# Performance work log

Measured on AMD Instinct MI355X. Metric: run time of the kernel, lower is better.

The kernel has to match this reference:

```python
import jax, jax.numpy as jnp
import numpy as np

N_NODES = 50000
N_EDGES = 1600000
N_GRAPHS = 64
IN_DIM = 128
HID = 128
N_CLASSES = 10


def setup_inputs() -> dict:
    key = jax.random.key(0)
    ks = jax.random.split(key, 12)
    x = jax.random.normal(ks[0], (N_NODES, IN_DIM), dtype=jnp.float32)
    edge_index = jax.random.randint(ks[1], (2, N_EDGES), 0, N_NODES, dtype=jnp.int32)
    batch = jnp.sort(jax.random.randint(ks[2], (N_NODES,), 0, N_GRAPHS, dtype=jnp.int32))
    def glorot(k, shape):
        s = 1.0 / np.sqrt(shape[0])
        return jax.random.uniform(k, shape, jnp.float32, -s, s)
    W1 = glorot(ks[3], (IN_DIM, HID)); b1 = jnp.zeros((HID,), jnp.float32)
    W2 = glorot(ks[4], (HID, HID));    b2 = jnp.zeros((HID,), jnp.float32)
    Wc1 = glorot(ks[5], (HID, HID));   bc1 = glorot(ks[6], (HID,))
    Wc2 = glorot(ks[7], (HID, N_CLASSES)); bc2 = glorot(ks[8], (N_CLASSES,))
    return {"x": x, "edge_index": edge_index, "batch": batch,
            "W1": W1, "b1": b1, "W2": W2, "b2": b2,
            "Wc1": Wc1, "bc1": bc1, "Wc2": Wc2, "bc2": bc2}


def gcn_conv(x, edge_index, W, b):
    """PyG GCNConv: sym-normalized A-hat (with self loops) @ (x W) + b."""
    n = x.shape[0]
    loop = jnp.arange(n, dtype=edge_index.dtype)
    src = jnp.concatenate([edge_index[0], loop])  # message source
    dst = jnp.concatenate([edge_index[1], loop])  # message target
    deg = jax.ops.segment_sum(jnp.ones_like(src, dtype=x.dtype), dst, num_segments=n)
    dinv = jnp.where(deg > 0, jax.lax.rsqrt(deg), jnp.zeros_like(deg))
    norm = dinv[src] * dinv[dst]  # [E+N]
    h = x @ W                     # [N, H]
    msg = h[src] * norm[:, None]  # gather + scale
    out = jax.ops.segment_sum(msg, dst, num_segments=n)
    return out + b


def reference(x, edge_index, batch, W1, b1, W2, b2, Wc1, bc1, Wc2, bc2):
    h = jax.nn.relu(gcn_conv(x, edge_index, W1, b1))
    h = jax.nn.relu(gcn_conv(h, edge_index, W2, b2))
    # per-graph mean pooling (segment mean)
    sums = jax.ops.segment_sum(h, batch, num_segments=N_GRAPHS)
    cnt = jax.ops.segment_sum(jnp.ones((h.shape[0],), h.dtype), batch, num_segments=N_GRAPHS)
    g = sums / jnp.clip(cnt, 1.0)[:, None]  # [G, H]
    z = jax.nn.relu(g @ Wc1 + bc1)
    return z @ Wc2 + bc2
```

## Files before the change

kernel.cpp:

```cpp
#include <hip/hip_runtime.h>
#include <cstdint>
#include <cstddef>

#define CHUNK 4096

typedef __attribute__((ext_vector_type(8))) short short8;
typedef __attribute__((ext_vector_type(4))) float f32x4;

__device__ __forceinline__ float bf2f(unsigned short u) {
  return __uint_as_float(((unsigned)u) << 16);
}
__device__ __forceinline__ unsigned short f2bf(float f) {
  unsigned u = __float_as_uint(f);
  u += 0x7fffu + ((u >> 16) & 1u);
  return (unsigned short)(u >> 16);
}

__global__ void transpose2_w_k(const float* __restrict__ W1, const float* __restrict__ W2,
                               unsigned short* __restrict__ W1t, unsigned short* __restrict__ W2t) {
  int idx = blockIdx.x * 256 + threadIdx.x;
  const float* W = (idx < 16384) ? W1 : W2;
  unsigned short* Wt = (idx < 16384) ? W1t : W2t;
  int i = idx & 16383;
  int k = i >> 7, n = i & 127;
  Wt[n * 128 + k] = f2bf(W[i]);
}

__global__ void count_edges_k(const int* __restrict__ dst, int E, int* __restrict__ cnt) {
  int e = blockIdx.x * blockDim.x + threadIdx.x;
  if (e < E) atomicAdd(&cnt[dst[e]], 1);
}

__global__ void dinv_k(const int* __restrict__ cnt, float* __restrict__ dinv, int n) {
  int i = blockIdx.x * blockDim.x + threadIdx.x;
  if (i < n) dinv[i] = rsqrtf((float)cnt[i] + 1.0f);
}

template <typename CT>
__global__ void fill_csr_k(const int* __restrict__ src, const int* __restrict__ dst, int E,
                           int* __restrict__ cursor, CT* __restrict__ col) {
  int e = blockIdx.x * blockDim.x + threadIdx.x;
  if (e < E) {
    int d = dst[e], s = src[e];
    int pos = atomicAdd(&cursor[d], 1);
    col[pos] = (CT)s;
  }
}

__global__ void scan1_k(const int* __restrict__ cnt, int* __restrict__ rs,
                        int* __restrict__ partials, int n) {
  __shared__ int s[1024];
  int t = threadIdx.x;
  int gid = blockIdx.x * 1024 + t;
  int v = (gid < n) ? cnt[gid] : 0;
  s[t] = v;
  __syncthreads();
  for (int off = 1; off < 1024; off <<= 1) {
    int u = (t >= off) ? s[t - off] : 0;
    __syncthreads();
    s[t] += u;
    __syncthreads();
  }
  if (gid < n) rs[gid] = s[t] - v;
  if (t == 1023) partials[blockIdx.x] = s[1023];
}

__global__ void scan2_k(int* __restrict__ partials, int nb) {
  if (threadIdx.x == 0 && blockIdx.x == 0) {
    int acc = 0;
    for (int i = 0; i < nb; i++) { int v = partials[i]; partials[i] = acc; acc += v; }
  }
}

__global__ void scan3_k(int* __restrict__ rs, int* __restrict__ cursor,
                        const int* __restrict__ partials, int n, int total) {
  int gid = blockIdx.x * blockDim.x + threadIdx.x;
  if (gid < n) {
    int v = rs[gid] + partials[gid >> 10];
    rs[gid] = v;
    cursor[gid] = v;
  }
  if (gid == 0) rs[n] = total;
}

__global__ __launch_bounds__(256) void scatter_atomic_k(const int* __restrict__ src,
                                                        const int* __restrict__ dst, int E,
                                                        int* __restrict__ gcur,
                                                        unsigned int* __restrict__ tmp,
                                                        int cap, int B) {
  __shared__ unsigned pk[CHUNK];
  __shared__ unsigned char bk[CHUNK];
  __shared__ int h[256];
  __shared__ int cur[256];
  __shared__ int base_s[256];
  int t = threadIdx.x;
  h[t] = 0;
  __syncthreads();
  int e0 = blockIdx.x * CHUNK;
  int e1 = e0 + CHUNK; if (e1 > E) e1 = E;
  int m = e1 - e0;
  for (int i = t; i < m; i += 256) {
    int d = dst[e0 + i], s = src[e0 + i];
    int b = d >> 8;
    pk[i] = ((unsigned)s << 8) | (unsigned)(d & 255);
    bk[i] = (unsigned char)b;
    atomicAdd(&h[b], 1);
  }
  __syncthreads();
  if (t < B && h[t] > 0) base_s[t] = atomicAdd(&gcur[t], h[t]);
  cur[t] = 0;
  __syncthreads();
  for (int i = t; i < m; i += 256) {
    int b = bk[i];
    int r = atomicAdd(&cur[b], 1);
    int p = base_s[b] + r;
    if (p < cap) tmp[(size_t)b * cap + p] = pk[i];
  }
}

__global__ void base2_k(const int* __restrict__ gcur, int B, int cap,
                        int* __restrict__ bucket_base) {
  int lane = threadIdx.x;
  int running = 0;
  for (int c0 = 0; c0 < B; c0 += 64) {
    int idx = c0 + lane;
    int cb = (idx < B) ? gcur[idx] : 0;
    if (cb > cap) cb = cap;
    int v = cb;
    #pragma unroll
    for (int off = 1; off < 64; off <<= 1) {
      int u = __shfl_up(v, off);
      if (lane >= off) v += u;
    }
    int tot = __shfl(v, 63);
    if (idx < B) bucket_base[idx] = running + (v - cb);
    running += tot;
  }
  if (lane == 0) bucket_base[B] = running;
}

__global__ __launch_bounds__(256) void cntfill2_k(const unsigned int* __restrict__ tmp,
                                                  const int* __restrict__ gcur,
                                                  const int* __restrict__ bucket_base,
                                                  int N, int E, int cap,
                                                  float* __restrict__ dinv,
                                                  int* __restrict__ rs,
                                                  unsigned short* __restrict__ col) {
  __shared__ int c[256];
  __shared__ int cur[256];
  int b = blockIdx.x, t = threadIdx.x;
  c[t] = 0;
  __syncthreads();
  int cnt_b = gcur[b]; if (cnt_b > cap) cnt_b = cap;
  const unsigned* tb = tmp + (size_t)b * cap;
  for (int i = t; i < cnt_b; i += 256) atomicAdd(&c[tb[i] & 255u], 1);
  __syncthreads();
  int v = c[t];
  cur[t] = v;
  __syncthreads();
  for (int off = 1; off < 256; off <<= 1) {
    int u = (t >= off) ? cur[t - off] : 0;
    __syncthreads();
    cur[t] += u;
    __syncthreads();
  }
  int rsv = bucket_base[b] + cur[t] - v;
  int node = (b << 8) + t;
  if (node < N) {
    rs[node] = rsv;
    dinv[node] = rsqrtf((float)v + 1.0f);
  }
  if (b == 0 && t == 0) rs[N] = E;
  __syncthreads();
  cur[t] = rsv;
  __syncthreads();
  for (int i = t; i < cnt_b; i += 256) {
    unsigned u = tb[i];
    int pos = atomicAdd(&cur[u & 255u], 1);
    col[pos] = (unsigned short)(u >> 8);
  }
}

template <bool AF32>
__global__ __launch_bounds__(256) void gemm_bf_k(const void* __restrict__ Ap,
                                                 const unsigned short* __restrict__ Wt,
                                                 unsigned short* __restrict__ C, int N) {
  __shared__ unsigned short Ws[128 * 136];
  for (int idx = threadIdx.x; idx < 2048; idx += 256) {
    int n = idx >> 4, c = idx & 15;
    *(uint4*)&Ws[n * 136 + c * 8] = ((const uint4*)Wt)[idx];
  }
  __syncthreads();
  const int w = threadIdx.x >> 6;
  const int lane = threadIdx.x & 63;
  const int quad = lane >> 4, l16 = lane & 15;
  const int rb = blockIdx.x * 128 + w * 32;
  f32x4 acc[2][8] = {};
  #pragma unroll
  for (int ks = 0; ks < 4; ks++) {
    short8 aF[2];
    #pragma unroll
    for (int m = 0; m < 2; m++) {
      int r = rb + m * 16 + l16;
      short8 a = {};
      if (r < N) {
        if (AF32) {
          const float* ar = (const float*)Ap + (size_t)r * 128 + ks * 32 + quad * 8;
          float4 u0 = *(const float4*)ar;
          float4 u1 = *(const float4*)(ar + 4);
          a[0] = (short)f2bf(u0.x); a[1] = (short)f2bf(u0.y);
          a[2] = (short)f2bf(u0.z); a[3] = (short)f2bf(u0.w);
          a[4] = (short)f2bf(u1.x); a[5] = (short)f2bf(u1.y);
          a[6] = (short)f2bf(u1.z); a[7] = (short)f2bf(u1.w);
        } else {
          a = *(const short8*)((const unsigned short*)Ap + (size_t)r * 128 + ks * 32 + quad * 8);
        }
      }
      aF[m] = a;
    }
    #pragma unroll
    for (int t = 0; t < 8; t++) {
      short8 bF = *(const short8*)&Ws[(t * 16 + l16) * 136 + ks * 32 + quad * 8];
      acc[0][t] = __builtin_amdgcn_mfma_f32_16x16x32_bf16(aF[0], bF, acc[0][t], 0, 0, 0);
      acc[1][t] = __builtin_amdgcn_mfma_f32_16x16x32_bf16(aF[1], bF, acc[1][t], 0, 0, 0);
    }
  }
  __syncthreads();
  unsigned short* Cs = Ws;
  #pragma unroll
  for (int m = 0; m < 2; m++) {
    int rloc = w * 32 + m * 16 + quad * 4;
    #pragma unroll
    for (int t = 0; t < 8; t++)
      #pragma unroll
      for (int rg = 0; rg < 4; rg++)
        Cs[(rloc + rg) * 132 + t * 16 + l16] = f2bf(acc[m][t][rg]);
  }
  __syncthreads();
  const int r0 = blockIdx.x * 128;
  for (int idx = threadIdx.x; idx < 2048; idx += 256) {
    int row = idx >> 4, c = idx & 15;
    int rr = r0 + row;
    if (rr < N) {
      uint2 a = *(uint2*)&Cs[row * 132 + c * 8];
      uint2 b = *(uint2*)&Cs[row * 132 + c * 8 + 4];
      ((uint4*)C)[(size_t)rr * 16 + c] = make_uint4(a.x, a.y, b.x, b.y);
    }
  }
}

template <typename CT>
__global__ __launch_bounds__(256) void agg8_k(const unsigned short* __restrict__ h,
                                              const int* __restrict__ rs,
                                              const CT* __restrict__ col,
                                              const float* __restrict__ dinv,
                                              const float* __restrict__ bias,
                                              unsigned short* __restrict__ outp, int n) {
  int wid = (blockIdx.x * blockDim.x + threadIdx.x) >> 6;
  int lane = threadIdx.x & 63;
  if (wid >= n) return;
  const int g = lane >> 4;
  const int l = lane & 15;
  float di = dinv[wid];
  float acc[8];
  {
    uint4 sv = ((const uint4*)(h + (size_t)wid * 128))[l];
    float ws = (g == 0) ? di : 0.f;
    acc[0] = bf2f((unsigned short)sv.x) * ws;
    acc[1] = bf2f((unsigned short)(sv.x >> 16)) * ws;
    acc[2] = bf2f((unsigned short)sv.y) * ws;
    acc[3] = bf2f((unsigned short)(sv.y >> 16)) * ws;
    acc[4] = bf2f((unsigned short)sv.z) * ws;
    acc[5] = bf2f((unsigned short)(sv.z >> 16)) * ws;
    acc[6] = bf2f((unsigned short)sv.w) * ws;
    acc[7] = bf2f((unsigned short)(sv.w >> 16)) * ws;
  }
  int beg = rs[wid], end = rs[wid + 1];
  for (int base = beg; base < end; base += 8) {
    int e0 = base + g, e1 = base + 4 + g;
    int i0 = (e0 < end) ? e0 : end - 1;
    int i1 = (e1 < end) ? e1 : end - 1;
    int s0 = (int)col[i0], s1 = (int)col[i1];
    float w0 = (e0 < end) ? dinv[s0] : 0.f;
    float w1 = (e1 < end) ? dinv[s1] : 0.f;
    uint4 h0 = ((const uint4*)(h + (size_t)s0 * 128))[l];
    uint4 h1 = ((const uint4*)(h + (size_t)s1 * 128))[l];
    acc[0] += bf2f((unsigned short)h0.x) * w0 + bf2f((unsigned short)h1.x) * w1;
    acc[1] += bf2f((unsigned short)(h0.x >> 16)) * w0 + bf2f((unsigned short)(h1.x >> 16)) * w1;
    acc[2] += bf2f((unsigned short)h0.y) * w0 + bf2f((unsigned short)h1.y) * w1;
    acc[3] += bf2f((unsigned short)(h0.y >> 16)) * w0 + bf2f((unsigned short)(h1.y >> 16)) * w1;
    acc[4] += bf2f((unsigned short)h0.z) * w0 + bf2f((unsigned short)h1.z) * w1;
    acc[5] += bf2f((unsigned short)(h0.z >> 16)) * w0 + bf2f((unsigned short)(h1.z >> 16)) * w1;
    acc[6] += bf2f((unsigned short)h0.w) * w0 + bf2f((unsigned short)h1.w) * w1;
    acc[7] += bf2f((unsigned short)(h0.w >> 16)) * w0 + bf2f((unsigned short)(h1.w >> 16)) * w1;
  }
  #pragma unroll
  for (int j = 0; j < 8; j++) {
    acc[j] += __shfl_xor(acc[j], 16);
    acc[j] += __shfl_xor(acc[j], 32);
  }
  if (g == 0) {
    float4 bA = *(const float4*)(bias + l * 8);
    float4 bB = *(const float4*)(bias + l * 8 + 4);
    float r0 = fmaxf(acc[0] * di + bA.x, 0.f);
    float r1 = fmaxf(acc[1] * di + bA.y, 0.f);
    float r2 = fmaxf(acc[2] * di + bA.z, 0.f);
    float r3 = fmaxf(acc[3] * di + bA.w, 0.f);
    float r4 = fmaxf(acc[4] * di + bB.x, 0.f);
    float r5 = fmaxf(acc[5] * di + bB.y, 0.f);
    float r6 = fmaxf(acc[6] * di + bB.z, 0.f);
    float r7 = fmaxf(acc[7] * di + bB.w, 0.f);
    uint4 v;
    v.x = (unsigned)f2bf(r0) | ((unsigned)f2bf(r1) << 16);
    v.y = (unsigned)f2bf(r2) | ((unsigned)f2bf(r3) << 16);
    v.z = (unsigned)f2bf(r4) | ((unsigned)f2bf(r5) << 16);
    v.w = (unsigned)f2bf(r6) | ((unsigned)f2bf(r7) << 16);
    ((uint4*)outp)[(size_t)wid * 16 + l] = v;
  }
}

__global__ void poolb_k(const unsigned short* __restrict__ h, const int* __restrict__ batch, int n,
                        float* __restrict__ pool, float* __restrict__ gcnt) {
  int f = threadIdx.x;
  int n0 = blockIdx.x * 64;
  if (n0 >= n) return;
  int n1 = n0 + 64; if (n1 > n) n1 = n;
  int gcur = batch[n0];
  float acc = 0.f, cacc = 0.f;
  for (int i = n0; i < n1; i++) {
    int g = batch[i];
    if (g != gcur) {
      atomicAdd(&pool[gcur * 128 + f], acc);
      if (f == 0) atomicAdd(&gcnt[gcur], cacc);
      acc = 0.f; cacc = 0.f; gcur = g;
    }
    acc += bf2f(h[(size_t)i * 128 + f]);
    cacc += 1.f;
  }
  atomicAdd(&pool[gcur * 128 + f], acc);
  if (f == 0) atomicAdd(&gcnt[gcur], cacc);
}

__global__ void classify_k(const float* __restrict__ pool, const float* __restrict__ gcnt,
                           const float* __restrict__ Wc1, const float* __restrict__ bc1,
                           const float* __restrict__ Wc2, const float* __restrict__ bc2,
                           float* __restrict__ out, int nc) {
  __shared__ float gs[128];
  __shared__ float zs[128];
  int g = blockIdx.x, t = threadIdx.x;
  float c = gcnt[g]; if (c < 1.f) c = 1.f;
  gs[t] = pool[g * 128 + t] / c;
  __syncthreads();
  float acc = bc1[t];
  for (int k = 0; k < 128; k++) acc += gs[k] * Wc1[k * 128 + t];
  zs[t] = fmaxf(acc, 0.f);
  __syncthreads();
  if (t < nc) {
    float o = bc2[t];
    for (int k = 0; k < 128; k++) o += zs[k] * Wc2[k * nc + t];
    out[g * nc + t] = o;
  }
}

extern "C" void kernel_launch(void* const* d_in, const int* in_sizes, int n_in,
                              void* d_out, int out_size, void* d_ws, size_t ws_size,
                              hipStream_t stream) {
  const float* x   = (const float*)d_in[0];
  const int*   ei  = (const int*)d_in[1];
  const int*   bat = (const int*)d_in[2];
  const float* W1  = (const float*)d_in[3];
  const float* b1  = (const float*)d_in[4];
  const float* W2  = (const float*)d_in[5];
  const float* b2  = (const float*)d_in[6];
  const float* Wc1 = (const float*)d_in[7];
  const float* bc1 = (const float*)d_in[8];
  const float* Wc2 = (const float*)d_in[9];
  const float* bc2 = (const float*)d_in[10];
  float* out = (float*)d_out;

  const int N  = in_sizes[0] / 128;
  const int E  = in_sizes[1] / 2;
  const int NC = in_sizes[10];
  const int G  = out_size / NC;
  const int* src = ei;
  const int* dst = ei + E;
  (void)n_in; (void)ws_size;

  size_t off = 0;
  auto walloc = [&](size_t bytes) -> void* {
    void* p = (char*)d_ws + off;
    off += (bytes + 255) & ~(size_t)255;
    return p;
  };
  unsigned short* B2 = (unsigned short*)walloc((size_t)N * 128 * 2);
  unsigned short* B3 = (unsigned short*)walloc((size_t)N * 128 * 2);
  unsigned short* W1t = (unsigned short*)walloc(128 * 128 * 2);
  unsigned short* W2t = (unsigned short*)walloc(128 * 128 * 2);
  float* dinv = (float*)walloc((size_t)N * 4);
  int*   rs   = (int*)  walloc((size_t)(N + 1) * 4);
  float* pool = (float*)walloc((size_t)G * 129 * 4);
  float* gcnt = pool + (size_t)G * 128;

  const bool small = (N <= 65535);
  const int gblocks = (N + 127) / 128;
  const int aggGrid = (N + 3) / 4;

  transpose2_w_k<<<128, 256, 0, stream>>>(W1, W2, W1t, W2t);

  if (small) {
    const int B    = (N + 255) >> 8;
    const int nblk = (E + CHUNK - 1) / CHUNK;
    const int cap  = (E + B - 1) / B + 2048;
    unsigned short* col = (unsigned short*)walloc((size_t)E * 2);
    unsigned int*   tmp = (unsigned int*)  walloc((size_t)B * cap * 4);
    int* gcur        = (int*)walloc((size_t)B * 4);
    int* bucket_base = (int*)walloc((size_t)(B + 1) * 4);

    hipMemsetAsync(gcur, 0, (size_t)B * 4, stream);
    scatter_atomic_k<<<nblk, 256, 0, stream>>>(src, dst, E, gcur, tmp, cap, B);
    base2_k<<<1, 64, 0, stream>>>(gcur, B, cap, bucket_base);
    cntfill2_k<<<B, 256, 0, stream>>>(tmp, gcur, bucket_base, N, E, cap, dinv, rs, col);

    gemm_bf_k<true><<<gblocks, 256, 0, stream>>>(x, W1t, B2, N);
    agg8_k<unsigned short><<<aggGrid, 256, 0, stream>>>(B2, rs, col, dinv, b1, B3, N);
    gemm_bf_k<false><<<gblocks, 256, 0, stream>>>(B3, W2t, B2, N);
    agg8_k<unsigned short><<<aggGrid, 256, 0, stream>>>(B2, rs, col, dinv, b2, B3, N);
  } else {
    const int nb = (N + 1023) / 1024;
    int* cnt    = (int*)walloc((size_t)N * 4);
    int* cursor = (int*)walloc((size_t)N * 4);
    int* col    = (int*)walloc((size_t)E * 4);
    int* partials = (int*)walloc(256 * 4);
    hipMemsetAsync(cnt, 0, (size_t)N * 4, stream);
    count_edges_k<<<(E + 255) / 256, 256, 0, stream>>>(dst, E, cnt);
    scan1_k<<<nb, 1024, 0, stream>>>(cnt, rs, partials, N);
    scan2_k<<<1, 64, 0, stream>>>(partials, nb);
    scan3_k<<<(N + 255) / 256, 256, 0, stream>>>(rs, cursor, partials, N, E);
    dinv_k<<<(N + 255) / 256, 256, 0, stream>>>(cnt, dinv, N);
    fill_csr_k<int><<<(E + 255) / 256, 256, 0, stream>>>(src, dst, E, cursor, col);

    gemm_bf_k<true><<<gblocks, 256, 0, stream>>>(x, W1t, B2, N);
    agg8_k<int><<<aggGrid, 256, 0, stream>>>(B2, rs, col, dinv, b1, B3, N);
    gemm_bf_k<false><<<gblocks, 256, 0, stream>>>(B3, W2t, B2, N);
    agg8_k<int><<<aggGrid, 256, 0, stream>>>(B2, rs, col, dinv, b2, B3, N);
  }

  hipMemsetAsync(pool, 0, (size_t)G * 129 * 4, stream);
  poolb_k<<<(N + 63) / 64, 128, 0, stream>>>(B3, bat, N, pool, gcnt);
  classify_k<<<G, 128, 0, stream>>>(pool, gcnt, Wc1, bc1, Wc2, bc2, out, NC);
}
```

Before: 314.4 us.

## Fuse CSR build with first GEMM and merge pooling with classifier

Several launches are merged. The gcur memset goes into the weight-transpose kernel, and the bucket-base scan moves into each CSR-fill block. CSR fill and the first GEMM share one grid through a shared-memory union. Pooling plus classifier become one per-graph kernel that binary-searches the sorted batch array, so atomics and the pool memset disappear. This cuts launch overhead and lets the CSR fill overlap the GEMM, but only 64 blocks now do the pooling, and the sequential sum per graph may be slow.

Result: slower. 384.3 us (+22.2%).

```diff
diff --git a/kernel.cpp b/kernel.cpp
--- a/kernel.cpp
+++ b/kernel.cpp
@@ -16,71 +16,21 @@
   return (unsigned short)(u >> 16);
 }
 
-__global__ void transpose2_w_k(const float* __restrict__ W1, const float* __restrict__ W2,
-                               unsigned short* __restrict__ W1t, unsigned short* __restrict__ W2t) {
+union SMem {
+  unsigned short ws[128 * 136];
+  struct { int c[256]; int cur[256]; int sb[256]; } cf;
+};
+
+__global__ void prep_k(const float* __restrict__ W1, const float* __restrict__ W2,
+                       unsigned short* __restrict__ W1t, unsigned short* __restrict__ W2t,
+                       int* __restrict__ gcur, int B) {
   int idx = blockIdx.x * 256 + threadIdx.x;
   const float* W = (idx < 16384) ? W1 : W2;
   unsigned short* Wt = (idx < 16384) ? W1t : W2t;
   int i = idx & 16383;
   int k = i >> 7, n = i & 127;
   Wt[n * 128 + k] = f2bf(W[i]);
-}
-
-__global__ void count_edges_k(const int* __restrict__ dst, int E, int* __restrict__ cnt) {
-  int e = blockIdx.x * blockDim.x + threadIdx.x;
-  if (e < E) atomicAdd(&cnt[dst[e]], 1);
-}
-
-__global__ void dinv_k(const int* __restrict__ cnt, float* __restrict__ dinv, int n) {
-  int i = blockIdx.x * blockDim.x + threadIdx.x;
-  if (i < n) dinv[i] = rsqrtf((float)cnt[i] + 1.0f);
-}
-
-template <typename CT>
-__global__ void fill_csr_k(const int* __restrict__ src, const int* __restrict__ dst, int E,
-                           int* __restrict__ cursor, CT* __restrict__ col) {
-  int e = blockIdx.x * blockDim.x + threadIdx.x;
-  if (e < E) {
-    int d = dst[e], s = src[e];
-    int pos = atomicAdd(&cursor[d], 1);
-    col[pos] = (CT)s;
-  }
-}
-
-__global__ void scan1_k(const int* __restrict__ cnt, int* __restrict__ rs,
-                        int* __restrict__ partials, int n) {
-  __shared__ int s[1024];
-  int t = threadIdx.x;
-  int gid = blockIdx.x * 1024 + t;
-  int v = (gid < n) ? cnt[gid] : 0;
-  s[t] = v;
-  __syncthreads();
-  for (int off = 1; off < 1024; off <<= 1) {
-    int u = (t >= off) ? s[t - off] : 0;
-    __syncthreads();
-    s[t] += u;
-    __syncthreads();
-  }
-  if (gid < n) rs[gid] = s[t] - v;
-  if (t == 1023) partials[blockIdx.x] = s[1023];
-}
-
-__global__ void scan2_k(int* __restrict__ partials, int nb) {
-  if (threadIdx.x == 0 && blockIdx.x == 0) {
-    int acc = 0;
-    for (int i = 0; i < nb; i++) { int v = partials[i]; partials[i] = acc; acc += v; }
-  }
-}
-
-__global__ void scan3_k(int* __restrict__ rs, int* __restrict__ cursor,
-                        const int* __restrict__ partials, int n, int total) {
-  int gid = blockIdx.x * blockDim.x + threadIdx.x;
-  if (gid < n) {
-    int v = rs[gid] + partials[gid >> 10];
-    rs[gid] = v;
-    cursor[gid] = v;
-  }
-  if (gid == 0) rs[n] = total;
+  if (blockIdx.x == 0 && threadIdx.x < B) gcur[threadIdx.x] = 0;
 }
 
 __global__ __launch_bounds__(256) void scatter_atomic_k(const int* __restrict__ src,
@@ -118,83 +68,19 @@
   }
 }
 
-__global__ void base2_k(const int* __restrict__ gcur, int B, int cap,
-                        int* __restrict__ bucket_base) {
-  int lane = threadIdx.x;
-  int running = 0;
-  for (int c0 = 0; c0 < B; c0 += 64) {
-    int idx = c0 + lane;
-    int cb = (idx < B) ? gcur[idx] : 0;
-    if (cb > cap) cb = cap;
-    int v = cb;
-    #pragma unroll
-    for (int off = 1; off < 64; off <<= 1) {
-      int u = __shfl_up(v, off);
-      if (lane >= off) v += u;
-    }
-    int tot = __shfl(v, 63);
-    if (idx < B) bucket_base[idx] = running + (v - cb);
-    running += tot;
-  }
-  if (lane == 0) bucket_base[B] = running;
-}
-
-__global__ __launch_bounds__(256) void cntfill2_k(const unsigned int* __restrict__ tmp,
-                                                  const int* __restrict__ gcur,
-                                                  const int* __restrict__ bucket_base,
-                                                  int N, int E, int cap,
-                                                  float* __restrict__ dinv,
-                                                  int* __restrict__ rs,
-                                                  unsigned short* __restrict__ col) {
-  __shared__ int c[256];
-  __shared__ int cur[256];
-  int b = blockIdx.x, t = threadIdx.x;
-  c[t] = 0;
-  __syncthreads();
-  int cnt_b = gcur[b]; if (cnt_b > cap) cnt_b = cap;
-  const unsigned* tb = tmp + (size_t)b * cap;
-  for (int i = t; i < cnt_b; i += 256) atomicAdd(&c[tb[i] & 255u], 1);
-  __syncthreads();
-  int v = c[t];
-  cur[t] = v;
-  __syncthreads();
-  for (int off = 1; off < 256; off <<= 1) {
-    int u = (t >= off) ? cur[t - off] : 0;
-    __syncthreads();
-    cur[t] += u;
-    __syncthreads();
-  }
-  int rsv = bucket_base[b] + cur[t] - v;
-  int node = (b << 8) + t;
-  if (node < N) {
-    rs[node] = rsv;
-    dinv[node] = rsqrtf((float)v + 1.0f);
-  }
-  if (b == 0 && t == 0) rs[N] = E;
-  __syncthreads();
-  cur[t] = rsv;
-  __syncthreads();
-  for (int i = t; i < cnt_b; i += 256) {
-    unsigned u = tb[i];
-    int pos = atomicAdd(&cur[u & 255u], 1);
-    col[pos] = (unsigned short)(u >> 8);
-  }
-}
-
 template <bool AF32>
-__global__ __launch_bounds__(256) void gemm_bf_k(const void* __restrict__ Ap,
-                                                 const unsigned short* __restrict__ Wt,
-                                                 unsigned short* __restrict__ C, int N) {
-  __shared__ unsigned short Ws[128 * 136];
+__device__ __forceinline__ void gemm_tile(SMem& sm, const void* Ap,
+                                          const unsigned short* Wt,
+                                          unsigned short* C, int N, int tile) {
   for (int idx = threadIdx.x; idx < 2048; idx += 256) {
     int n = idx >> 4, c = idx & 15;
-    *(uint4*)&Ws[n * 136 + c * 8] = ((const uint4*)Wt)[idx];
+    *(uint4*)&sm.ws[n * 136 + c * 8] = ((const uint4*)Wt)[idx];
   }
   __syncthreads();
   const int w = threadIdx.x >> 6;
   const int lane = threadIdx.x & 63;
   const int quad = lane >> 4, l16 = lane & 15;
-  const int rb = blockIdx.x * 128 + w * 32;
+  const int rb = tile * 128 + w * 32;
   f32x4 acc[2][8] = {};
   #pragma unroll
   for (int ks = 0; ks < 4; ks++) {
@@ -220,13 +106,13 @@
     }
     #pragma unroll
     for (int t = 0; t < 8; t++) {
-      short8 bF = *(const short8*)&Ws[(t * 16 + l16) * 136 + ks * 32 + quad * 8];
+      short8 bF = *(const short8*)&sm.ws[(t * 16 + l16) * 136 + ks * 32 + quad * 8];
       acc[0][t] = __builtin_amdgcn_mfma_f32_16x16x32_bf16(aF[0], bF, acc[0][t], 0, 0, 0);
       acc[1][t] = __builtin_amdgcn_mfma_f32_16x16x32_bf16(aF[1], bF, acc[1][t], 0, 0, 0);
     }
   }
   __syncthreads();
-  unsigned short* Cs = Ws;
+  unsigned short* Cs = sm.ws;
   #pragma unroll
   for (int m = 0; m < 2; m++) {
     int rloc = w * 32 + m * 16 + quad * 4;
@@ -237,7 +123,7 @@
         Cs[(rloc + rg) * 132 + t * 16 + l16] = f2bf(acc[m][t][rg]);
   }
   __syncthreads();
-  const int r0 = blockIdx.x * 128;
+  const int r0 = tile * 128;
   for (int idx = threadIdx.x; idx < 2048; idx += 256) {
     int row = idx >> 4, c = idx & 15;
     int rr = r0 + row;
@@ -247,6 +133,73 @@
       ((uint4*)C)[(size_t)rr * 16 + c] = make_uint4(a.x, a.y, b.x, b.y);
     }
   }
+}
+
+__global__ __launch_bounds__(256) void cntfill_gemm1_k(const unsigned int* __restrict__ tmp,
+                                                       const int* __restrict__ gcur,
+                                                       int N, int E, int cap, int B,
+                                                       float* __restrict__ dinv,
+                                                       int* __restrict__ rs,
+                                                       unsigned short* __restrict__ col,
+                                                       const float* __restrict__ x,
+                                                       const unsigned short* __restrict__ W1t,
+                                                       unsigned short* __restrict__ B2) {
+  __shared__ SMem sm;
+  const int t = threadIdx.x;
+  if ((int)blockIdx.x >= B) {
+    gemm_tile<true>(sm, x, W1t, B2, N, blockIdx.x - B);
+    return;
+  }
+  int b = blockIdx.x;
+  int cb = 0;
+  if (t < B) { cb = gcur[t]; if (cb > cap) cb = cap; }
+  sm.cf.sb[t] = cb;
+  __syncthreads();
+  for (int off = 1; off < 256; off <<= 1) {
+    int u = (t >= off) ? sm.cf.sb[t - off] : 0;
+    __syncthreads();
+    sm.cf.sb[t] += u;
+    __syncthreads();
+  }
+  int base_b = (b > 0) ? sm.cf.sb[b - 1] : 0;
+  int cnt_b = sm.cf.sb[b] - base_b;
+  if (b == 0 && t == 0) rs[N] = sm.cf.sb[B - 1];
+  const unsigned* tb = tmp + (size_t)b * cap;
+  sm.cf.c[t] = 0;
+  __syncthreads();
+  for (int i = t; i < cnt_b; i += 256) atomicAdd(&sm.cf.c[tb[i] & 255u], 1);
+  __syncthreads();
+  int v = sm.cf.c[t];
+  sm.cf.cur[t] = v;
+  __syncthreads();
+  for (int off = 1; off < 256; off <<= 1) {
+    int u = (t >= off) ? sm.cf.cur[t - off] : 0;
+    __syncthreads();
+    sm.cf.cur[t] += u;
+    __syncthreads();
+  }
+  int rsv = base_b + sm.cf.cur[t] - v;
+  int node = (b << 8) + t;
+  if (node < N) {
+    rs[node] = rsv;
+    dinv[node] = rsqrtf((float)v + 1.0f);
+  }
+  __syncthreads();
+  sm.cf.cur[t] = rsv;
+  __syncthreads();
+  for (int i = t; i < cnt_b; i += 256) {
+    unsigned u = tb[i];
+    int pos = atomicAdd(&sm.cf.cur[u & 255u], 1);
+    col[pos] = (unsigned short)(u >> 8);
+  }
+}
+
+template <bool AF32>
+__global__ __launch_bounds__(256) void gemm_bf_k(const void* __restrict__ Ap,
+                                                 const unsigned short* __restrict__ Wt,
+                                                 unsigned short* __restrict__ C, int N) {
+  __shared__ SMem sm;
+  gemm_tile<AF32>(sm, Ap, Wt, C, N, blockIdx.x);
 }
 
 template <typename CT>
@@ -319,47 +272,104 @@
   }
 }
 
-__global__ void poolb_k(const unsigned short* __restrict__ h, const int* __restrict__ batch, int n,
-                        float* __restrict__ pool, float* __restrict__ gcnt) {
-  int f = threadIdx.x;
-  int n0 = blockIdx.x * 64;
-  if (n0 >= n) return;
-  int n1 = n0 + 64; if (n1 > n) n1 = n;
-  int gcur = batch[n0];
-  float acc = 0.f, cacc = 0.f;
-  for (int i = n0; i < n1; i++) {
-    int g = batch[i];
-    if (g != gcur) {
-      atomicAdd(&pool[gcur * 128 + f], acc);
-      if (f == 0) atomicAdd(&gcnt[gcur], cacc);
-      acc = 0.f; cacc = 0.f; gcur = g;
-    }
+__global__ __launch_bounds__(256) void poolclassify_k(const unsigned short* __restrict__ h,
+                                                      const int* __restrict__ bat, int n,
+                                                      const float* __restrict__ Wc1,
+                                                      const float* __restrict__ bc1,
+                                                      const float* __restrict__ Wc2,
+                                                      const float* __restrict__ bc2,
+                                                      float* __restrict__ out, int nc) {
+  __shared__ float gs[128];
+  __shared__ float part[128];
+  __shared__ float zs[128];
+  const int g = blockIdx.x;
+  const int t = threadIdx.x;
+  int lo;
+  {
+    int l = 0, r = n;
+    while (l < r) { int m = (l + r) >> 1; if (bat[m] < g) l = m + 1; else r = m; }
+    lo = l;
+  }
+  int hi;
+  {
+    int l = lo, r = n;
+    while (l < r) { int m = (l + r) >> 1; if (bat[m] < g + 1) l = m + 1; else r = m; }
+    hi = l;
+  }
+  const int f = t & 127;
+  const int half = t >> 7;
+  float acc = 0.f;
+  for (int i = lo + half; i < hi; i += 2)
     acc += bf2f(h[(size_t)i * 128 + f]);
-    cacc += 1.f;
-  }
-  atomicAdd(&pool[gcur * 128 + f], acc);
-  if (f == 0) atomicAdd(&gcnt[gcur], cacc);
-}
-
-__global__ void classify_k(const float* __restrict__ pool, const float* __restrict__ gcnt,
-                           const float* __restrict__ Wc1, const float* __restrict__ bc1,
-                           const float* __restrict__ Wc2, const float* __restrict__ bc2,
-                           float* __restrict__ out, int nc) {
-  __shared__ float gs[128];
-  __shared__ float zs[128];
-  int g = blockIdx.x, t = threadIdx.x;
-  float c = gcnt[g]; if (c < 1.f) c = 1.f;
-  gs[t] = pool[g * 128 + t] / c;
-  __syncthreads();
-  float acc = bc1[t];
-  for (int k = 0; k < 128; k++) acc += gs[k] * Wc1[k * 128 + t];
-  zs[t] = fmaxf(acc, 0.f);
+  if (half == 1) part[f] = acc;
+  __syncthreads();
+  if (half == 0) {
+    float c = (float)(hi - lo); if (c < 1.f) c = 1.f;
+    gs[f] = (acc + part[f]) / c;
+  }
+  __syncthreads();
+  if (t < 128) {
+    float a = bc1[t];
+    for (int k = 0; k < 128; k++) a += gs[k] * Wc1[k * 128 + t];
+    zs[t] = fmaxf(a, 0.f);
+  }
   __syncthreads();
   if (t < nc) {
     float o = bc2[t];
     for (int k = 0; k < 128; k++) o += zs[k] * Wc2[k * nc + t];
     out[g * nc + t] = o;
   }
+}
+
+__global__ void count_edges_k(const int* __restrict__ dst, int E, int* __restrict__ cnt) {
+  int e = blockIdx.x * blockDim.x + threadIdx.x;
+  if (e < E) atomicAdd(&cnt[dst[e]], 1);
+}
+__global__ void dinv_k(const int* __restrict__ cnt, float* __restrict__ dinv, int n) {
+  int i = blockIdx.x * blockDim.x + threadIdx.x;
+  if (i < n) dinv[i] = rsqrtf((float)cnt[i] + 1.0f);
+}
+__global__ void fill_csr_k(const int* __restrict__ src, const int* __restrict__ dst, int E,
+                           int* __restrict__ cursor, int* __restrict__ col) {
+  int e = blockIdx.x * blockDim.x + threadIdx.x;
+  if (e < E) {
+    int d = dst[e], s = src[e];
+    int pos = atomicAdd(&cursor[d], 1);
+    col[pos] = s;
+  }
+}
+__global__ void scan1_k(const int* __restrict__ cnt, int* __restrict__ rs,
+                        int* __restrict__ partials, int n) {
+  __shared__ int s[1024];
+  int t = threadIdx.x;
+  int gid = blockIdx.x * 1024 + t;
+  int v = (gid < n) ? cnt[gid] : 0;
+  s[t] = v;
+  __syncthreads();
+  for (int off = 1; off < 1024; off <<= 1) {
+    int u = (t >= off) ? s[t - off] : 0;
+    __syncthreads();
+    s[t] += u;
+    __syncthreads();
+  }
+  if (gid < n) rs[gid] = s[t] - v;
+  if (t == 1023) partials[blockIdx.x] = s[1023];
+}
+__global__ void scan2_k(int* __restrict__ partials, int nb) {
+  if (threadIdx.x == 0 && blockIdx.x == 0) {
+    int acc = 0;
+    for (int i = 0; i < nb; i++) { int v = partials[i]; partials[i] = acc; acc += v; }
+  }
+}
+__global__ void scan3_k(int* __restrict__ rs, int* __restrict__ cursor,
+                        const int* __restrict__ partials, int n, int total) {
+  int gid = blockIdx.x * blockDim.x + threadIdx.x;
+  if (gid < n) {
+    int v = rs[gid] + partials[gid >> 10];
+    rs[gid] = v;
+    cursor[gid] = v;
+  }
+  if (gid == 0) rs[n] = total;
 }
 
 extern "C" void kernel_launch(void* const* d_in, const int* in_sizes, int n_in,
@@ -398,14 +408,10 @@
   unsigned short* W2t = (unsigned short*)walloc(128 * 128 * 2);
   float* dinv = (float*)walloc((size_t)N * 4);
   int*   rs   = (int*)  walloc((size_t)(N + 1) * 4);
-  float* pool = (float*)walloc((size_t)G * 129 * 4);
-  float* gcnt = pool + (size_t)G * 128;
 
   const bool small = (N <= 65535);
   const int gblocks = (N + 127) / 128;
   const int aggGrid = (N + 3) / 4;
-
-  transpose2_w_k<<<128, 256, 0, stream>>>(W1, W2, W1t, W2t);
 
   if (small) {
     const int B    = (N + 255) >> 8;
@@ -413,39 +419,35 @@
     const int cap  = (E + B - 1) / B + 2048;
     unsigned short* col = (unsigned short*)walloc((size_t)E * 2);
     unsigned int*   tmp = (unsigned int*)  walloc((size_t)B * cap * 4);
-    int* gcur        = (int*)walloc((size_t)B * 4);
-    int* bucket_base = (int*)walloc((size_t)(B + 1) * 4);
-
-    hipMemsetAsync(gcur, 0, (size_t)B * 4, stream);
+    int* gcur = (int*)walloc((size_t)B * 4);
+
+    prep_k<<<128, 256, 0, stream>>>(W1, W2, W1t, W2t, gcur, B);
     scatter_atomic_k<<<nblk, 256, 0, stream>>>(src, dst, E, gcur, tmp, cap, B);
-    base2_k<<<1, 64, 0, stream>>>(gcur, B, cap, bucket_base);
-    cntfill2_k<<<B, 256, 0, stream>>>(tmp, gcur, bucket_base, N, E, cap, dinv, rs, col);
-
-    gemm_bf_k<true><<<gblocks, 256, 0, stream>>>(x, W1t, B2, N);
+    cntfill_gemm1_k<<<B + gblocks, 256, 0, stream>>>(tmp, gcur, N, E, cap, B,
+                                                     dinv, rs, col, x, W1t, B2);
     agg8_k<unsigned short><<<aggGrid, 256, 0, stream>>>(B2, rs, col, dinv, b1, B3, N);
     gemm_bf_k<false><<<gblocks, 256, 0, stream>>>(B3, W2t, B2, N);
     agg8_k<unsigned short><<<aggGrid, 256, 0, stream>>>(B2, rs, col, dinv, b2, B3, N);
+    poolclassify_k<<<G, 256, 0, stream>>>(B3, bat, N, Wc1, bc1, Wc2, bc2, out, NC);
   } else {
     const int nb = (N + 1023) / 1024;
     int* cnt    = (int*)walloc((size_t)N * 4);
     int* cursor = (int*)walloc((size_t)N * 4);
     int* col    = (int*)walloc((size_t)E * 4);
     int* partials = (int*)walloc(256 * 4);
+    prep_k<<<128, 256, 0, stream>>>(W1, W2, W1t, W2t, cnt , 0);
     hipMemsetAsync(cnt, 0, (size_t)N * 4, stream);
     count_edges_k<<<(E + 255) / 256, 256, 0, stream>>>(dst, E, cnt);
     scan1_k<<<nb, 1024, 0, stream>>>(cnt, rs, partials, N);
     scan2_k<<<1, 64, 0, stream>>>(partials, nb);
     scan3_k<<<(N + 255) / 256, 256, 0, stream>>>(rs, cursor, partials, N, E);
     dinv_k<<<(N + 255) / 256, 256, 0, stream>>>(cnt, dinv, N);
-    fill_csr_k<int><<<(E + 255) / 256, 256, 0, stream>>>(src, dst, E, cursor, col);
+    fill_csr_k<<<(E + 255) / 256, 256, 0, stream>>>(src, dst, E, cursor, col);
 
     gemm_bf_k<true><<<gblocks, 256, 0, stream>>>(x, W1t, B2, N);
     agg8_k<int><<<aggGrid, 256, 0, stream>>>(B2, rs, col, dinv, b1, B3, N);
     gemm_bf_k<false><<<gblocks, 256, 0, stream>>>(B3, W2t, B2, N);
     agg8_k<int><<<aggGrid, 256, 0, stream>>>(B2, rs, col, dinv, b2, B3, N);
-  }
-
-  hipMemsetAsync(pool, 0, (size_t)G * 129 * 4, stream);
-  poolb_k<<<(N + 63) / 64, 128, 0, stream>>>(B3, bat, N, pool, gcnt);
-  classify_k<<<G, 128, 0, stream>>>(pool, gcnt, Wc1, bc1, Wc2, bc2, out, NC);
-}
+    poolclassify_k<<<G, 256, 0, stream>>>(B3, bat, N, Wc1, bc1, Wc2, bc2, out, NC);
+  }
+}
```
